# Kernel optimization log

Measured on AMD Instinct MI355X. Metric: run time of the kernel, lower is better.

## Reference

```python
import jax, jax.numpy as jnp
import numpy as np

K = 16  # kNN neighbors (KnnEncoder default)


def _bn(h, g, s):
    # eval-mode BatchNorm with running mean 0 / var 1 folded into affine
    return h * g + s


def setup_inputs() -> dict:
    key = jax.random.key(0)
    cnt = [0]
    def nk():
        cnt[0] += 1
        return jax.random.fold_in(key, cnt[0])
    B, N = 4, 4096
    def W(i, o):
        return jax.random.normal(nk(), (i, o), jnp.float32) / np.float32(i) ** 0.5
    def bias(d):
        return jnp.zeros((d,), jnp.float32)
    def gamma(d):
        return jnp.ones((d,), jnp.float32) + 0.1 * jax.random.normal(nk(), (d,), jnp.float32)
    def beta(d):
        return 0.1 * jax.random.normal(nk(), (d,), jnp.float32)
    inp = dict(
        pos=jax.random.normal(nk(), (B, N, 3), jnp.float32),
        query_point_idx=jax.random.randint(nk(), (B,), 0, N),
        # PointNetConv local MLP: 6 -> 64 -> 128 -> 256 (plain last)
        cw1=W(6, 64), cb1=bias(64), cg1=gamma(64), cs1=beta(64),
        cw2=W(64, 128), cb2=bias(128), cg2=gamma(128), cs2=beta(128),
        cw3=W(128, 256), cb3=bias(256),
        # GlobalSAModule MLP: 259 -> 256 -> 512 -> 1024 (plain last)
        sw1=W(259, 256), sb1=bias(256), sg1=gamma(256), ss1=beta(256),
        sw2=W(256, 512), sb2=bias(512), sg2=gamma(512), ss2=beta(512),
        sw3=W(512, 1024), sb3=bias(1024),
        # EdgeGraspPredictor: 1280 -> 512 -> 256 -> 16
        pw1=W(1280, 512), pb1=bias(512),
        pw2=W(512, 256), pb2=bias(256),
        pw3=W(256, 16), pb3=bias(16),
    )
    return inp


def reference(pos, query_point_idx, cw1, cb1, cg1, cs1, cw2, cb2, cg2, cs2, cw3, cb3,
              sw1, sb1, sg1, ss1, sw2, sb2, sg2, ss2, sw3, sb3,
              pw1, pb1, pw2, pb2, pw3, pb3):
    B, N, _ = pos.shape
    # kNN within each cloud (self included, as torch_geometric knn with x==y)
    d2 = jnp.sum((pos[:, :, None, :] - pos[:, None, :, :]) ** 2, axis=-1)  # [B,N,N]
    _, idx = jax.lax.top_k(-d2, K)  # [B,N,K] targets for each source point n
    nbr = jax.vmap(lambda p, i: p[i])(pos, idx)  # [B,N,K,3] target positions
    # PointNetConv message: cat([x_j = pos_src, pos_src - pos_tgt])
    src = jnp.broadcast_to(pos[:, :, None, :], (B, N, K, 3))
    h = jnp.concatenate([src, src - nbr], axis=-1)  # [B,N,K,6]
    h = jnp.maximum(_bn(h @ cw1 + cb1, cg1, cs1), 0.0)
    h = jnp.maximum(_bn(h @ cw2 + cb2, cg2, cs2), 0.0)
    m = h @ cw3 + cb3  # [B,N,K,256] per-edge messages
    # scatter-max aggregation at target nodes (every node has its self edge)
    tgt = (idx + (jnp.arange(B) * N)[:, None, None]).reshape(-1)
    x = jax.ops.segment_max(m.reshape(-1, m.shape[-1]), tgt, num_segments=B * N)
    x = x.reshape(B, N, -1)  # [B,N,256] per-point features
    # GlobalSAModule: pointwise MLP then global max pool per cloud
    g = jnp.concatenate([x, pos], axis=-1)  # [B,N,259]
    g = jnp.maximum(_bn(g @ sw1 + sb1, sg1, ss1), 0.0)
    g = jnp.maximum(_bn(g @ sw2 + sb2, sg2, ss2), 0.0)
    g = g @ sw3 + sb3  # [B,N,1024]
    scene = jnp.max(g, axis=1)  # [B,1024]
    # gather query point feature, concat with scene feature, predictor MLP
    q = query_point_idx + jnp.arange(B) * N
    point_feat = x.reshape(B * N, -1)[q]  # [B,256]
    ef = jnp.concatenate([point_feat, scene], axis=-1)  # [B,1280]
    h = jnp.maximum(ef @ pw1 + pb1, 0.0)
    h = jnp.maximum(h @ pw2 + pb2, 0.0)
    return h @ pw3 + pb3  # [B,16]
```

## Files before the change

### kernel.cpp

```cpp
#include <hip/hip_runtime.h>

#define BB 4
#define NN 4096
#define KK 16

typedef unsigned short u16;
typedef unsigned int   u32;
typedef unsigned long long u64;

typedef __attribute__((ext_vector_type(8))) short bf16x8;
typedef __attribute__((ext_vector_type(4))) float f32x4;

__device__ __forceinline__ float b2f(u16 x){ return __uint_as_float(((u32)x) << 16); }
__device__ __forceinline__ u16 f2b(float f){
    u32 u = __float_as_uint(f);
    u32 r = (u + 0x7FFFu + ((u >> 16) & 1u)) >> 16;
    return (u16)r;
}
__device__ __forceinline__ u32 fmap(float f){
    u32 u = __float_as_uint(f);
    return (u & 0x80000000u) ? ~u : (u | 0x80000000u);
}
__device__ __forceinline__ float funmap(u32 u){
    u32 v = (u & 0x80000000u) ? (u ^ 0x80000000u) : ~u;
    return __uint_as_float(v);
}

#define N_ARR 27
__device__ const int ASZ[N_ARR] = {
    49152, 384, 64, 64, 64, 8192, 128, 128, 128, 32768, 256,
    66304, 256, 256, 256, 131072, 512, 512, 512, 524288, 1024,
    655360, 512, 131072, 256, 4096, 16 };
__device__ const int AOFF[N_ARR] = {
    0, 49152, 49536, 49600, 49664, 49728, 57920, 58048, 58176, 58304, 91072,
    91328, 157632, 157888, 158144, 158400, 289472, 289984, 290496, 291008, 815296,
    816320, 1471680, 1472192, 1603264, 1603520, 1607616 };

struct Ptrs { const void* p[N_ARR]; };

#define O_POS 0
#define O_CW1 49152
#define O_CB1 49536
#define O_CG1 49600
#define O_CS1 49664
#define O_CB2 57920
#define O_CG2 58048
#define O_CS2 58176
#define O_CB3 91072
#define O_SW1 91328
#define O_SB1 157632
#define O_SG1 157888
#define O_SS1 158144
#define O_SB2 289472
#define O_SG2 289984
#define O_SS2 290496
#define O_SB3 815296
#define O_PW1 816320
#define O_PB1 1471680
#define O_PW2 1472192
#define O_PB2 1603264
#define O_PW3 1603520
#define O_PB3 1607616

__global__ void detect_kernel(const u16* __restrict__ pos_u16, u32* __restrict__ flag){
    __shared__ int cnt;
    if (threadIdx.x == 0) cnt = 0;
    __syncthreads();
    int c = 0;
    #pragma unroll
    for (int s = 0; s < 4; ++s){
        u16 u = pos_u16[2*(threadIdx.x*4 + s)];
        int e = (u >> 7) & 0xFF;
        c += (e >= 0x68 && e <= 0x82) ? 1 : 0;
    }
    atomicAdd(&cnt, c);
    __syncthreads();
    if (threadIdx.x == 0) *flag = (cnt >= 512) ? 1u : 0u;
}

__device__ __forceinline__ void pack_one_src(const void* __restrict__ src, bool isbf,
                                             u16* __restrict__ dst, int tot, int log2n,
                                             int g, int T){
    const int nmask = (1 << log2n) - 1;
    for (int id = g; id < tot; id += T){
        int i = id & 7, lg = (id >> 3) & 3;
        int rest = id >> 5;
        int n = rest & nmask;
        int ks = rest >> log2n;
        int si = (ks*32 + lg*8 + i) << log2n | n;
        dst[id] = isbf ? ((const u16*)src)[si] : f2b(((const float*)src)[si]);
    }
}

__global__ __launch_bounds__(256) void prep_kernel(Ptrs pt, const u32* __restrict__ flagp,
        float* __restrict__ dst, float* __restrict__ psoa,
        u16* __restrict__ wp2, u16* __restrict__ wp3,
        u16* __restrict__ swp1, u16* __restrict__ swp2, u16* __restrict__ swp3){
    const bool isbf = (*flagp != 0);
    const int T = gridDim.x * 256;
    const int g = blockIdx.x * 256 + threadIdx.x;
    #pragma unroll
    for (int a = 0; a < N_ARR; ++a){
        if (a == 5 || a == 9 || a == 15 || a == 19) continue;
        const int sz = ASZ[a], off = AOFF[a];
        if (isbf){
            const u16* s = (const u16*)pt.p[a];
            for (int i = g; i < sz; i += T) dst[off + i] = b2f(s[i]);
        } else {
            const float* s = (const float*)pt.p[a];
            for (int i = g; i < sz; i += T) dst[off + i] = s[i];
        }
    }
    for (int i = g; i < BB*NN; i += T){
        float x, y, z;
        if (isbf){
            const u16* s = (const u16*)pt.p[0];
            x = b2f(s[3*i]); y = b2f(s[3*i+1]); z = b2f(s[3*i+2]);
        } else {
            const float* s = (const float*)pt.p[0];
            x = s[3*i]; y = s[3*i+1]; z = s[3*i+2];
        }
        psoa[i] = x; psoa[BB*NN + i] = y; psoa[2*BB*NN + i] = z;
    }
    pack_one_src(pt.p[5],  isbf, wp2,    8192,  7, g, T);
    pack_one_src(pt.p[9],  isbf, wp3,   32768,  8, g, T);
    pack_one_src(pt.p[11], isbf, swp1,  65536,  8, g, T);
    pack_one_src(pt.p[15], isbf, swp2, 131072,  9, g, T);
    pack_one_src(pt.p[19], isbf, swp3, 524288, 10, g, T);
}

__global__ __launch_bounds__(1024) void sort1_kernel(const float* __restrict__ psoa,
                                                     u64* __restrict__ keys){
    __shared__ u64 s[2048];
    const int half = blockIdx.x;
    const int b    = half >> 1;
    const int base = (half & 1) << 11;
    const float* px = psoa + b*NN;
    const int tid = threadIdx.x;
    for (int i = tid; i < 2048; i += 1024)
        s[i] = (((u64)fmap(px[base + i])) << 32) | (u32)(base + i);
    __syncthreads();
    for (int ksz = 2; ksz <= 2048; ksz <<= 1){
        for (int jj = ksz >> 1; jj > 0; jj >>= 1){
            int t = tid;
            int i  = ((t & ~(jj-1)) << 1) | (t & (jj-1));
            int ix = i | jj;
            u64 a = s[i], v = s[ix];
            bool up = (((base + i) & ksz) == 0);
            if ((a > v) == up){ s[i] = v; s[ix] = a; }
            __syncthreads();
        }
    }
    for (int i = tid; i < 2048; i += 1024) keys[b*NN + base + i] = s[i];
}

__global__ __launch_bounds__(1024) void sort2_kernel(const u64* __restrict__ keys,
        const float* __restrict__ psoa,
        float* __restrict__ xs, float* __restrict__ ys, float* __restrict__ zs,
        int* __restrict__ sidx){
    __shared__ u64 s[NN];
    const int b = blockIdx.x;
    const int tid = threadIdx.x;
    for (int i = tid; i < NN; i += 1024) s[i] = keys[b*NN + i];
    __syncthreads();
    for (int jj = NN >> 1; jj > 0; jj >>= 1){
        for (int t = tid; t < NN/2; t += 1024){
            int i  = ((t & ~(jj-1)) << 1) | (t & (jj-1));
            int ix = i | jj;
            u64 a = s[i], v = s[ix];
            if (a > v){ s[i] = v; s[ix] = a; }
        }
        __syncthreads();
    }
    const float* py = psoa + BB*NN;
    const float* pz = psoa + 2*BB*NN;
    for (int r = tid; r < NN; r += 1024){
        u64 kv = s[r];
        int oi = (int)(u32)(kv & 0xFFFFFFFFu);
        xs[b*NN + r] = funmap((u32)(kv >> 32));
        ys[b*NN + r] = py[b*NN + oi];
        zs[b*NN + r] = pz[b*NN + oi];
        sidx[b*NN + r] = oi;
    }
}

#define QCAP 192
__device__ __forceinline__ void refine16(u64* __restrict__ buf, int& cnt, float& tau, int lane){
    u64 loc[3];
    #pragma unroll
    for (int q = 0; q < 3; ++q){
        int p = lane + (q << 6);
        loc[q] = (p < cnt) ? buf[p] : ~0ull;
    }
    u64 m = ~0ull;
    #pragma unroll
    for (int r = 0; r < KK; ++r){
        m = loc[0];
        m = loc[1] < m ? loc[1] : m;
        m = loc[2] < m ? loc[2] : m;
        #pragma unroll
        for (int off = 32; off > 0; off >>= 1){
            u64 o = __shfl_xor(m, off);
            m = o < m ? o : m;
        }
        if (lane == r) buf[r] = m;
        #pragma unroll
        for (int q = 0; q < 3; ++q) if (loc[q] == m) loc[q] = ~0ull;
    }
    cnt = KK;
    tau = __uint_as_float((u32)(m >> 32));
}

__global__ __launch_bounds__(512) void knn_kernel(
        const float* __restrict__ xs, const float* __restrict__ ys,
        const float* __restrict__ zs, const int* __restrict__ sidx,
        int* __restrict__ knn_out, u32* __restrict__ deg){
    __shared__ __align__(16) u64 kbuf[16*QCAP];
    const int b  = blockIdx.x >> 8;
    const int r0 = (blockIdx.x & 255) << 4;
    const float* X = xs + b*NN;
    const float* Y = ys + b*NN;
    const float* Z = zs + b*NN;
    const int*   S = sidx + b*NN;
    const int tid = threadIdx.x;
    const int lane = tid & 63;
    const int wv = tid >> 6;
    const int rA = r0 + wv*2, rB = rA + 1;
    const float axq = X[rA], ayq = Y[rA], azq = Z[rA];
    const float bxq = X[rB], byq = Y[rB], bzq = Z[rB];
    u64* bufA = kbuf + (wv*2)*QCAP;
    u64* bufB = bufA + QCAP;

    float tauA = 3.0e38f, tauB = 3.0e38f;
    int cntA = 0, cntB = 0;
    for (int k = 0; k < 128; ++k){
        int j = (lane < 32) ? (rA - 1 - (k << 5) - lane)
                            : (rA + (k << 5) + (lane - 32));
        bool inr = ((u32)j < (u32)NN);
        int ja = inr ? j : rA;
        float cx = X[ja], cy = Y[ja], cz = Z[ja];
        float dxA = axq - cx, dyA = ayq - cy, dzA = azq - cz;
        float d2A = __fadd_rn(__fadd_rn(__fmul_rn(dxA,dxA), __fmul_rn(dyA,dyA)), __fmul_rn(dzA,dzA));
        float dxB = bxq - cx, dyB = byq - cy, dzB = bzq - cz;
        float d2B = __fadd_rn(__fadd_rn(__fmul_rn(dxB,dxB), __fmul_rn(dyB,dyB)), __fmul_rn(dzB,dzB));
        bool pA = inr && (d2A <= tauA);
        bool pB = inr && (d2B <= tauB);
        u64 balA = __ballot(pA);
        u64 balB = __ballot(pB);
        int sorig = 0;
        if (balA | balB) sorig = S[ja];
        if (balA){
            int nins = __popcll(balA);
            if (cntA + nins > QCAP) refine16(bufA, cntA, tauA, lane);
            if (pA){
                int ofs = __popcll(balA & ((1ull << lane) - 1ull));
                bufA[cntA + ofs] = (((u64)__float_as_uint(d2A)) << 32) | (u32)sorig;
            }
            cntA += nins;
        }
        if (balB){
            int nins = __popcll(balB);
            if (cntB + nins > QCAP) refine16(bufB, cntB, tauB, lane);
            if (pB){
                int ofs = __popcll(balB & ((1ull << lane) - 1ull));
                bufB[cntB + ofs] = (((u64)__float_as_uint(d2B)) << 32) | (u32)sorig;
            }
            cntB += nins;
        }
        float xL = __shfl(cx, 31);
        float xR = __shfl(cx, 63);
        bool lex = (rA - ((k + 1) << 5) - 1) < 0;
        bool rex = (rA + ((k + 1) << 5)) >= NN;
        float dLa = axq - xL, dRa = xR - axq;
        float dLb = bxq - xL, dRb = xR - bxq;
        bool ldone = lex || (dLa*dLa > tauA && dLb*dLb > tauB);
        bool rdone = rex || (dRa*dRa > tauA && dRb*dRb > tauB);
        if (ldone && rdone) break;
    }
    refine16(bufA, cntA, tauA, lane);
    refine16(bufB, cntB, tauB, lane);
    const int origA = S[rA], origB = S[rB];
    if (lane < KK){
        u64 kA = bufA[lane];
        int jA = (int)(u32)(kA & 0xFFFFFFFFu);
        knn_out[((size_t)(b*NN + origA))*KK + lane] = jA;
        atomicAdd(deg + (b << 12) + jA, 1u);
        u64 kB = bufB[lane];
        int jB = (int)(u32)(kB & 0xFFFFFFFFu);
        knn_out[((size_t)(b*NN + origB))*KK + lane] = jB;
        atomicAdd(deg + (b << 12) + jB, 1u);
    }
}

__global__ __launch_bounds__(1024) void scan_kernel(const u32* __restrict__ deg,
                                                    int* __restrict__ rowstart, u32* __restrict__ cursor){
    __shared__ int lsum[1024];
    const int tid = threadIdx.x;
    const int base = tid * 16;
    int loc[16]; int s = 0;
    #pragma unroll
    for (int q = 0; q < 16; ++q){ loc[q] = (int)deg[base+q]; s += loc[q]; }
    lsum[tid] = s;
    __syncthreads();
    int acc = s;
    for (int ofs = 1; ofs < 1024; ofs <<= 1){
        int t = (tid >= ofs) ? lsum[tid-ofs] : 0;
        __syncthreads();
        acc += t; lsum[tid] = acc;
        __syncthreads();
    }
    int excl = acc - s;
    #pragma unroll
    for (int q = 0; q < 16; ++q){
        rowstart[base+q] = excl; cursor[base+q] = (u32)excl; excl += loc[q];
    }
    if (tid == 1023) rowstart[16384] = excl;
}

__global__ __launch_bounds__(256) void fill_kernel(const int* __restrict__ knn,
                                                   u32* __restrict__ cursor, int* __restrict__ csr){
    int e = blockIdx.x*256 + threadIdx.x;
    int b = e >> 16;
    int t = (b << 12) + knn[e];
    u32 pos = atomicAdd(cursor + t, 1u);
    csr[pos] = e;
}

__device__ __forceinline__ bf16x8 ldfrag(const u16* h, int row, int kofs, int rowstride){
    u32 byte = (u32)((row*rowstride + kofs)*2) ^ (u32)((row & 7) << 4);
    return *(const bf16x8*)((const char*)h + byte);
}
__device__ __forceinline__ void st16(u16* h, int row, int col, int rowstride, float v){
    u32 byte = (u32)((row*rowstride + col)*2) ^ (u32)((row & 7) << 4);
    *(u16*)((char*)h + byte) = f2b(v);
}

__global__ __launch_bounds__(256, 2) void edge_kernel(
    const float* __restrict__ conv, const int* __restrict__ knn,
    const int* __restrict__ rowstart, const int* __restrict__ csr,
    const u16* __restrict__ wp2, const u16* __restrict__ wp3,
    u16* __restrict__ xh)
{
    __shared__ float in6[6][64];
    __shared__ int   lts[64];
    __shared__ int   rs_l[17];
    __shared__ float scw1[384];
    __shared__ float sc1[64], sh1[64];
    __shared__ __align__(16) u16 h1s[64*64];
    __shared__ __align__(16) u16 h2s[64*128];
    __shared__ u32 lsx[16*256];

    const float* posf = conv + O_POS;
    const float* cb1 = conv + O_CB1; const float* cg1 = conv + O_CG1; const float* cs1 = conv + O_CS1;

    const int tid = threadIdx.x;
    const int w   = tid >> 6;
    const int l   = tid & 63;
    const int t0  = blockIdx.x << 4;
    const int b   = t0 >> 12;

    if (tid < 64){ float g1 = cg1[tid]; sc1[tid]=g1; sh1[tid]=cb1[tid]*g1 + cs1[tid]; }
    if (tid < 17) rs_l[tid] = rowstart[t0 + tid];
    for (int u = tid; u < 384; u += 256) scw1[u] = conv[O_CW1 + u];
    #pragma unroll
    for (int q = 0; q < 16; ++q) lsx[q*256 + tid] = 0u;

    const int lr = l & 15, lg = l >> 4;
    const int colb2 = w << 5;
    const int colb3 = w << 6;

    float sc2v[2], sh2v[2], bs3v[4];
    #pragma unroll
    for (int nt = 0; nt < 2; ++nt){
        int c = colb2 + nt*16 + lr;
        float g2 = conv[O_CG2 + c];
        sc2v[nt] = g2; sh2v[nt] = conv[O_CB2 + c]*g2 + conv[O_CS2 + c];
    }
    #pragma unroll
    for (int nt = 0; nt < 4; ++nt) bs3v[nt] = conv[O_CB3 + colb3 + nt*16 + lr];

    __syncthreads();
    const int segstart = rs_l[0], segend = rs_l[16];
    const int nchunk = (segend - segstart + 63) >> 6;

    int curl = -1;
    float run[4];
    #pragma unroll
    for (int nt = 0; nt < 4; ++nt) run[nt] = 0.f;

    for (int ch = 0; ch < nchunk; ++ch){
        __syncthreads();
        if (tid < 64){
            int gpos = segstart + (ch << 6) + tid;
            int lt = -1;
            float ax=0,ay=0,az=0,dx=0,dy=0,dz=0;
            if (gpos < segend){
                lt = 0;
                #pragma unroll
                for (int q = 1; q < 16; ++q) lt += (gpos >= rs_l[q]) ? 1 : 0;
                int e = csr[gpos];
                int i = (e >> 4) & (NN - 1);
                int j = knn[e];
                const float* pi = posf + ((size_t)(b*NN + i))*3;
                const float* pj = posf + ((size_t)(b*NN + j))*3;
                ax = pi[0]; ay = pi[1]; az = pi[2];
                dx = ax - pj[0]; dy = ay - pj[1]; dz = az - pj[2];
            }
            lts[tid] = lt;
            in6[0][tid]=ax; in6[1][tid]=ay; in6[2][tid]=az;
            in6[3][tid]=dx; in6[4][tid]=dy; in6[5][tid]=dz;
        }
        __syncthreads();

        {
            const int e = tid & 63, c0g = (tid >> 6) << 4;
            float a0=in6[0][e], a1=in6[1][e], a2=in6[2][e],
                  a3=in6[3][e], a4=in6[4][e], a5=in6[5][e];
            u32 pk[8];
            #pragma unroll
            for (int ci = 0; ci < 16; ++ci){
                int cc = c0g + ci;
                float acc = a0*scw1[cc]     + a1*scw1[64+cc]  + a2*scw1[128+cc]
                          + a3*scw1[192+cc] + a4*scw1[256+cc] + a5*scw1[320+cc];
                float v = fmaxf(acc*sc1[cc] + sh1[cc], 0.f);
                u32 h = (u32)f2b(v);
                if (ci & 1) pk[ci >> 1] |= h << 16; else pk[ci >> 1] = h;
            }
            u32 base = (u32)(e*128 + c0g*2);
            u32 swz  = (u32)((e & 7) << 4);
            *(uint4*)((char*)h1s + (base ^ swz))        = make_uint4(pk[0],pk[1],pk[2],pk[3]);
            *(uint4*)((char*)h1s + ((base + 16) ^ swz)) = make_uint4(pk[4],pk[5],pk[6],pk[7]);
        }
        __syncthreads();

        {
            f32x4 acc2[4][2];
            #pragma unroll
            for (int mt = 0; mt < 4; ++mt)
                #pragma unroll
                for (int nt = 0; nt < 2; ++nt) acc2[mt][nt] = (f32x4){0.f,0.f,0.f,0.f};
            #pragma unroll
            for (int ks = 0; ks < 2; ++ks){
                bf16x8 bf[2];
                #pragma unroll
                for (int nt = 0; nt < 2; ++nt)
                    bf[nt] = *(const bf16x8*)(wp2 + (((ks*128 + colb2 + nt*16 + lr) << 2) + lg)*8);
                #pragma unroll
                for (int mt = 0; mt < 4; ++mt){
                    bf16x8 a = ldfrag(h1s, mt*16 + lr, ks*32 + lg*8, 64);
                    #pragma unroll
                    for (int nt = 0; nt < 2; ++nt)
                        acc2[mt][nt] = __builtin_amdgcn_mfma_f32_16x16x32_bf16(a, bf[nt], acc2[mt][nt], 0, 0, 0);
                }
            }
            #pragma unroll
            for (int mt = 0; mt < 4; ++mt)
                #pragma unroll
                for (int nt = 0; nt < 2; ++nt)
                    #pragma unroll
                    for (int r = 0; r < 4; ++r){
                        int row = mt*16 + lg*4 + r;
                        float v = fmaxf(acc2[mt][nt][r]*sc2v[nt] + sh2v[nt], 0.f);
                        st16(h2s, row, colb2 + nt*16 + lr, 128, v);
                    }
        }
        __syncthreads();

        {
            f32x4 acc3[4][4];
            #pragma unroll
            for (int mt = 0; mt < 4; ++mt)
                #pragma unroll
                for (int nt = 0; nt < 4; ++nt) acc3[mt][nt] = (f32x4){0.f,0.f,0.f,0.f};
            #pragma unroll
            for (int ks = 0; ks < 4; ++ks){
                bf16x8 bf[4];
                #pragma unroll
                for (int nt = 0; nt < 4; ++nt)
                    bf[nt] = *(const bf16x8*)(wp3 + (((ks*256 + colb3 + nt*16 + lr) << 2) + lg)*8);
                #pragma unroll
                for (int mt = 0; mt < 4; ++mt){
                    bf16x8 a = ldfrag(h2s, mt*16 + lr, ks*32 + lg*8, 128);
                    #pragma unroll
                    for (int nt = 0; nt < 4; ++nt)
                        acc3[mt][nt] = __builtin_amdgcn_mfma_f32_16x16x32_bf16(a, bf[nt], acc3[mt][nt], 0, 0, 0);
                }
            }
            #pragma unroll
            for (int mt = 0; mt < 4; ++mt)
                #pragma unroll
                for (int r = 0; r < 4; ++r){
                    int row = mt*16 + lg*4 + r;
                    int lt = lts[row];
                    if (lt != curl){
                        if (curl >= 0){
                            #pragma unroll
                            for (int nt = 0; nt < 4; ++nt)
                                atomicMax(&lsx[curl*256 + colb3 + nt*16 + lr], fmap(run[nt]));
                        }
                        curl = lt;
                        #pragma unroll
                        for (int nt = 0; nt < 4; ++nt) run[nt] = acc3[mt][nt][r] + bs3v[nt];
                    } else {
                        #pragma unroll
                        for (int nt = 0; nt < 4; ++nt) run[nt] = fmaxf(run[nt], acc3[mt][nt][r] + bs3v[nt]);
                    }
                }
        }
    }
    if (curl >= 0){
        #pragma unroll
        for (int nt = 0; nt < 4; ++nt)
            atomicMax(&lsx[curl*256 + colb3 + nt*16 + lr], fmap(run[nt]));
    }
    __syncthreads();
    #pragma unroll
    for (int q = 0; q < 16; ++q)
        xh[((size_t)(t0+q))*256 + tid] = f2b(funmap(lsx[q*256 + tid]));
}

__global__ __launch_bounds__(256, 3) void sa_kernel(
    const float* __restrict__ conv, const u16* __restrict__ xh,
    const u16* __restrict__ swp1, const u16* __restrict__ swp2, const u16* __restrict__ swp3,
    u32* __restrict__ scene_map)
{
    __shared__ __align__(16) u16 h1s[32*256];
    __shared__ __align__(16) u16 h2s[32*512];
    __shared__ float spw[3][256];
    __shared__ float spx[32], spy[32], spz[32];

    const int tid = threadIdx.x;
    const int w   = tid >> 6;
    const int l   = tid & 63;
    const int lr  = l & 15, lg = l >> 4;
    const int b   = blockIdx.x >> 7;
    const int n0  = (blockIdx.x & 127) << 5;
    const u16* xrow = xh + ((size_t)(b*NN + n0))*256;

    if (tid < 96){
        int p = tid & 31, d = tid >> 5;
        float v = conv[O_POS + ((size_t)(b*NN + n0 + p))*3 + d];
        if (d == 0) spx[p] = v; else if (d == 1) spy[p] = v; else spz[p] = v;
    }
    for (int u = tid; u < 768; u += 256)
        spw[u >> 8][u & 255] = conv[O_SW1 + (256 + (u >> 8))*256 + (u & 255)];
    __syncthreads();

    {
        const int c0 = w << 6;
        float sc1v[4], sh1v[4];
        #pragma unroll
        for (int nt = 0; nt < 4; ++nt){
            int cc = c0 + nt*16 + lr;
            float g = conv[O_SG1 + cc];
            sc1v[nt] = g; sh1v[nt] = conv[O_SB1 + cc]*g + conv[O_SS1 + cc];
        }
        f32x4 acc[2][4];
        #pragma unroll
        for (int mt = 0; mt < 2; ++mt)
            #pragma unroll
            for (int nt = 0; nt < 4; ++nt)
                #pragma unroll
                for (int r = 0; r < 4; ++r){
                    int row = mt*16 + lg*4 + r;
                    int cc  = c0 + nt*16 + lr;
                    acc[mt][nt][r] = spx[row]*spw[0][cc] + spy[row]*spw[1][cc] + spz[row]*spw[2][cc];
                }
        #pragma unroll
        for (int ks = 0; ks < 8; ++ks){
            bf16x8 bf[4];
            #pragma unroll
            for (int nt = 0; nt < 4; ++nt)
                bf[nt] = *(const bf16x8*)(swp1 + (((ks*256 + c0 + nt*16 + lr) << 2) + lg)*8);
            #pragma unroll
            for (int mt = 0; mt < 2; ++mt){
                bf16x8 a = *(const bf16x8*)(xrow + (mt*16 + lr)*256 + ks*32 + lg*8);
                #pragma unroll
                for (int nt = 0; nt < 4; ++nt)
                    acc[mt][nt] = __builtin_amdgcn_mfma_f32_16x16x32_bf16(a, bf[nt], acc[mt][nt], 0, 0, 0);
            }
        }
        #pragma unroll
        for (int mt = 0; mt < 2; ++mt)
            #pragma unroll
            for (int nt = 0; nt < 4; ++nt)
                #pragma unroll
                for (int r = 0; r < 4; ++r){
                    int row = mt*16 + lg*4 + r;
                    float v = fmaxf(acc[mt][nt][r]*sc1v[nt] + sh1v[nt], 0.f);
                    st16(h1s, row, c0 + nt*16 + lr, 256, v);
                }
    }
    __syncthreads();

    {
        const int c0 = w << 7;
        float sc2v[8], sh2v[8];
        #pragma unroll
        for (int nt = 0; nt < 8; ++nt){
            int cc = c0 + nt*16 + lr;
            float g = conv[O_SG2 + cc];
            sc2v[nt] = g; sh2v[nt] = conv[O_SB2 + cc]*g + conv[O_SS2 + cc];
        }
        f32x4 acc[2][8];
        #pragma unroll
        for (int mt = 0; mt < 2; ++mt)
            #pragma unroll
            for (int nt = 0; nt < 8; ++nt) acc[mt][nt] = (f32x4){0.f,0.f,0.f,0.f};
        #pragma unroll
        for (int ks = 0; ks < 8; ++ks){
            bf16x8 bf[8];
            #pragma unroll
            for (int nt = 0; nt < 8; ++nt)
                bf[nt] = *(const bf16x8*)(swp2 + (((ks*512 + c0 + nt*16 + lr) << 2) + lg)*8);
            #pragma unroll
            for (int mt = 0; mt < 2; ++mt){
                bf16x8 a = ldfrag(h1s, mt*16 + lr, ks*32 + lg*8, 256);
                #pragma unroll
                for (int nt = 0; nt < 8; ++nt)
                    acc[mt][nt] = __builtin_amdgcn_mfma_f32_16x16x32_bf16(a, bf[nt], acc[mt][nt], 0, 0, 0);
            }
        }
        #pragma unroll
        for (int mt = 0; mt < 2; ++mt)
            #pragma unroll
            for (int nt = 0; nt < 8; ++nt)
                #pragma unroll
                for (int r = 0; r < 4; ++r){
                    int row = mt*16 + lg*4 + r;
                    float v = fmaxf(acc[mt][nt][r]*sc2v[nt] + sh2v[nt], 0.f);
                    st16(h2s, row, c0 + nt*16 + lr, 512, v);
                }
    }
    __syncthreads();

    #pragma unroll
    for (int half = 0; half < 2; ++half){
        const int c0 = (half << 9) + (w << 7);
        f32x4 acc[2][8];
        #pragma unroll
        for (int mt = 0; mt < 2; ++mt)
            #pragma unroll
            for (int nt = 0; nt < 8; ++nt) acc[mt][nt] = (f32x4){0.f,0.f,0.f,0.f};
        #pragma unroll
        for (int ks = 0; ks < 16; ++ks){
            bf16x8 bf[8];
            #pragma unroll
            for (int nt = 0; nt < 8; ++nt)
                bf[nt] = *(const bf16x8*)(swp3 + (((ks*1024 + c0 + nt*16 + lr) << 2) + lg)*8);
            #pragma unroll
            for (int mt = 0; mt < 2; ++mt){
                bf16x8 a = ldfrag(h2s, mt*16 + lr, ks*32 + lg*8, 512);
                #pragma unroll
                for (int nt = 0; nt < 8; ++nt)
                    acc[mt][nt] = __builtin_amdgcn_mfma_f32_16x16x32_bf16(a, bf[nt], acc[mt][nt], 0, 0, 0);
            }
        }
        #pragma unroll
        for (int nt = 0; nt < 8; ++nt){
            float v = acc[0][nt][0];
            #pragma unroll
            for (int mt = 0; mt < 2; ++mt)
                #pragma unroll
                for (int r = 0; r < 4; ++r) v = fmaxf(v, acc[mt][nt][r]);
            v = fmaxf(v, __shfl_xor(v, 16));
            v = fmaxf(v, __shfl_xor(v, 32));
            if (lg == 0){
                int cc = c0 + nt*16 + lr;
                atomicMax(scene_map + (b << 10) + cc, fmap(v + conv[O_SB3 + cc]));
            }
        }
    }
}

__global__ __launch_bounds__(128) void head1_kernel(
    const float* __restrict__ conv,
    const u16* __restrict__ xh, const u32* __restrict__ scene_map, const int* __restrict__ qidx,
    float* __restrict__ h1out)
{
    __shared__ float ef[1280];
    __shared__ float psum[4][32];
    const float* pw1 = conv + O_PW1; const float* pb1 = conv + O_PB1;
    const int b  = blockIdx.x >> 4;
    const int c0 = (blockIdx.x & 15) << 5;
    const int tid = threadIdx.x;
    const int q = qidx[b];
    for (int u = tid; u < 1280; u += 128){
        float v;
        if (u < 256) v = b2f(xh[(((size_t)(b*NN + q)) << 8) + u]);
        else         v = funmap(scene_map[(b << 10) + (u - 256)]);
        ef[u] = v;
    }
    __syncthreads();
    const int c = c0 + (tid & 31);
    const int rc = tid >> 5;
    float acc = 0.f;
    for (int r = rc*320; r < rc*320 + 320; ++r) acc += ef[r] * pw1[r*512 + c];
    psum[rc][tid & 31] = acc;
    __syncthreads();
    if (tid < 32){
        float a = psum[0][tid] + psum[1][tid] + psum[2][tid] + psum[3][tid] + pb1[c0 + tid];
        h1out[(b << 9) + c0 + tid] = fmaxf(a, 0.f);
    }
}

__global__ __launch_bounds__(256) void head2_kernel(
    const float* __restrict__ conv, const float* __restrict__ h1in,
    const u32* __restrict__ flagp, void* __restrict__ outv)
{
    __shared__ float h1[4][512];
    __shared__ float h2[4][256];
    const float* pw2 = conv + O_PW2; const float* pb2 = conv + O_PB2;
    const float* pw3 = conv + O_PW3; const float* pb3 = conv + O_PB3;
    const int tid = threadIdx.x;
    for (int u = tid; u < 2048; u += 256) h1[u >> 9][u & 511] = h1in[u];
    __syncthreads();
    for (int o = tid; o < 1024; o += 256){
        int b = o >> 8, c = o & 255;
        float acc = pb2[c];
        for (int r = 0; r < 512; ++r) acc += h1[b][r] * pw2[r*256 + c];
        h2[b][c] = fmaxf(acc, 0.f);
    }
    __syncthreads();
    if (tid < 64){
        int b = tid >> 4, c = tid & 15;
        float acc = pb3[c];
        for (int r = 0; r < 256; ++r) acc += h2[b][r] * pw3[r*16 + c];
        if (*flagp) ((u16*)outv)[tid] = f2b(acc);
        else        ((float*)outv)[tid] = acc;
    }
}

extern "C" void kernel_launch(void* const* d_in, const int* in_sizes, int n_in,
                              void* d_out, int out_size, void* d_ws, size_t ws_size,
                              hipStream_t stream){
    (void)in_sizes; (void)n_in; (void)out_size; (void)ws_size;
    const int* qidx = (const int*)d_in[1];

    char* ws = (char*)d_ws;
    u32*  flag      = (u32*)ws;
    float* conv     = (float*)(ws + 1024);
    u16*  wp2       = (u16*)(ws + 6432768);
    u16*  wp3       = (u16*)(ws + 6449152);
    u16*  swp1      = (u16*)(ws + 6514688);
    u16*  swp2      = (u16*)(ws + 6645760);
    u16*  swp3      = (u16*)(ws + 6907904);
    int*  knn       = (int*)(ws + 7956480);
    u32*  deg       = (u32*)(ws + 9005056);
    u32*  scene_map = (u32*)(ws + 9070592);
    int*  rowstart  = (int*)(ws + 9086976);
    u32*  cursor    = (u32*)(ws + 9152576);
    int*  csr       = (int*)(ws + 9218112);
    u16*  xh        = (u16*)(ws + 10266688);
    float* h1ws     = (float*)(ws + 18655296);
    float* psoa     = (float*)(ws + 18663488);
    float* xs       = (float*)(ws + 18860096);
    float* ys       = (float*)(ws + 18925632);
    float* zs       = (float*)(ws + 18991168);
    int*   sidx     = (int*)(ws + 19056704);
    u64*   keys     = (u64*)(ws + 19122240);

    Ptrs pt;
    pt.p[0] = d_in[0];
    for (int k = 1; k < N_ARR; ++k) pt.p[k] = d_in[k + 1];

    hipMemsetAsync(ws + 9005056, 0, 81920, stream);

    detect_kernel <<<1, 256, 0, stream>>>((const u16*)d_in[0], flag);
    prep_kernel   <<<512, 256, 0, stream>>>(pt, flag, conv, psoa, wp2, wp3, swp1, swp2, swp3);
    sort1_kernel  <<<BB*2, 1024, 0, stream>>>(psoa, keys);
    sort2_kernel  <<<BB, 1024, 0, stream>>>(keys, psoa, xs, ys, zs, sidx);
    knn_kernel <<<1024, 512, 0, stream>>>(xs, ys, zs, sidx, knn, deg);
    scan_kernel<<<1, 1024, 0, stream>>>(deg, rowstart, cursor);
    fill_kernel<<<1024, 256, 0, stream>>>(knn, cursor, csr);
    edge_kernel<<<1024, 256, 0, stream>>>(conv, knn, rowstart, csr, wp2, wp3, xh);
    sa_kernel  <<<512, 256, 0, stream>>>(conv, xh, swp1, swp2, swp3, scene_map);
    head1_kernel<<<64, 128, 0, stream>>>(conv, xh, scene_map, qidx, h1ws);
    head2_kernel<<<1, 256, 0, stream>>>(conv, h1ws, flag, (void*)d_out);
}
```

Before: 384.1 us.

## Batch kNN candidate loads per 8 steps and halve SA kernel row tile

The kNN scan now loads 8 candidate chunks of coordinates up front before processing them, so global load latency overlaps instead of stalling on each iteration. The early-exit check now runs only every 8 chunks, so some wasted distance work past the stopping point is possible. The SA kernel tile shrinks from 32 to 16 points per block, doubling the grid to 1024 blocks and raising the occupancy hint to 4 blocks per SIMD-group. This lowers register and LDS use, but each weight fragment is now reused over half as many rows, so weight reads from L2 roughly double.

```diff
diff --git a/kernel.cpp b/kernel.cpp
--- a/kernel.cpp
+++ b/kernel.cpp
@@ -233,42 +233,56 @@
 
     float tauA = 3.0e38f, tauB = 3.0e38f;
     int cntA = 0, cntB = 0;
-    for (int k = 0; k < 128; ++k){
-        int j = (lane < 32) ? (rA - 1 - (k << 5) - lane)
-                            : (rA + (k << 5) + (lane - 32));
-        bool inr = ((u32)j < (u32)NN);
-        int ja = inr ? j : rA;
-        float cx = X[ja], cy = Y[ja], cz = Z[ja];
-        float dxA = axq - cx, dyA = ayq - cy, dzA = azq - cz;
-        float d2A = __fadd_rn(__fadd_rn(__fmul_rn(dxA,dxA), __fmul_rn(dyA,dyA)), __fmul_rn(dzA,dzA));
-        float dxB = bxq - cx, dyB = byq - cy, dzB = bzq - cz;
-        float d2B = __fadd_rn(__fadd_rn(__fmul_rn(dxB,dxB), __fmul_rn(dyB,dyB)), __fmul_rn(dzB,dzB));
-        bool pA = inr && (d2A <= tauA);
-        bool pB = inr && (d2B <= tauB);
-        u64 balA = __ballot(pA);
-        u64 balB = __ballot(pB);
-        int sorig = 0;
-        if (balA | balB) sorig = S[ja];
-        if (balA){
-            int nins = __popcll(balA);
-            if (cntA + nins > QCAP) refine16(bufA, cntA, tauA, lane);
-            if (pA){
-                int ofs = __popcll(balA & ((1ull << lane) - 1ull));
-                bufA[cntA + ofs] = (((u64)__float_as_uint(d2A)) << 32) | (u32)sorig;
-            }
-            cntA += nins;
-        }
-        if (balB){
-            int nins = __popcll(balB);
-            if (cntB + nins > QCAP) refine16(bufB, cntB, tauB, lane);
-            if (pB){
-                int ofs = __popcll(balB & ((1ull << lane) - 1ull));
-                bufB[cntB + ofs] = (((u64)__float_as_uint(d2B)) << 32) | (u32)sorig;
-            }
-            cntB += nins;
-        }
-        float xL = __shfl(cx, 31);
-        float xR = __shfl(cx, 63);
+    for (int k0 = 0; k0 < 128; k0 += 8){
+        float cxv[8], cyv[8], czv[8];
+        #pragma unroll
+        for (int c = 0; c < 8; ++c){
+            int k = k0 + c;
+            int j = (lane < 32) ? (rA - 1 - (k << 5) - lane)
+                                : (rA + (k << 5) + (lane - 32));
+            int ja = ((u32)j < (u32)NN) ? j : rA;
+            cxv[c] = X[ja]; cyv[c] = Y[ja]; czv[c] = Z[ja];
+        }
+        #pragma unroll
+        for (int c = 0; c < 8; ++c){
+            int k = k0 + c;
+            int j = (lane < 32) ? (rA - 1 - (k << 5) - lane)
+                                : (rA + (k << 5) + (lane - 32));
+            bool inr = ((u32)j < (u32)NN);
+            int ja = inr ? j : rA;
+            float cx = cxv[c], cy = cyv[c], cz = czv[c];
+            float dxA = axq - cx, dyA = ayq - cy, dzA = azq - cz;
+            float d2A = __fadd_rn(__fadd_rn(__fmul_rn(dxA,dxA), __fmul_rn(dyA,dyA)), __fmul_rn(dzA,dzA));
+            float dxB = bxq - cx, dyB = byq - cy, dzB = bzq - cz;
+            float d2B = __fadd_rn(__fadd_rn(__fmul_rn(dxB,dxB), __fmul_rn(dyB,dyB)), __fmul_rn(dzB,dzB));
+            bool pA = inr && (d2A <= tauA);
+            bool pB = inr && (d2B <= tauB);
+            u64 balA = __ballot(pA);
+            u64 balB = __ballot(pB);
+            int sorig = 0;
+            if (balA | balB) sorig = S[ja];
+            if (balA){
+                int nins = __popcll(balA);
+                if (cntA + nins > QCAP) refine16(bufA, cntA, tauA, lane);
+                if (pA){
+                    int ofs = __popcll(balA & ((1ull << lane) - 1ull));
+                    bufA[cntA + ofs] = (((u64)__float_as_uint(d2A)) << 32) | (u32)sorig;
+                }
+                cntA += nins;
+            }
+            if (balB){
+                int nins = __popcll(balB);
+                if (cntB + nins > QCAP) refine16(bufB, cntB, tauB, lane);
+                if (pB){
+                    int ofs = __popcll(balB & ((1ull << lane) - 1ull));
+                    bufB[cntB + ofs] = (((u64)__float_as_uint(d2B)) << 32) | (u32)sorig;
+                }
+                cntB += nins;
+            }
+        }
+        float xL = __shfl(cxv[7], 31);
+        float xR = __shfl(cxv[7], 63);
+        const int k = k0 + 7;
         bool lex = (rA - ((k + 1) << 5) - 1) < 0;
         bool rex = (rA + ((k + 1) << 5)) >= NN;
         float dLa = axq - xL, dRa = xR - axq;
@@ -519,26 +533,26 @@
         xh[((size_t)(t0+q))*256 + tid] = f2b(funmap(lsx[q*256 + tid]));
 }
 
-__global__ __launch_bounds__(256, 3) void sa_kernel(
+__global__ __launch_bounds__(256, 4) void sa_kernel(
     const float* __restrict__ conv, const u16* __restrict__ xh,
     const u16* __restrict__ swp1, const u16* __restrict__ swp2, const u16* __restrict__ swp3,
     u32* __restrict__ scene_map)
 {
-    __shared__ __align__(16) u16 h1s[32*256];
-    __shared__ __align__(16) u16 h2s[32*512];
+    __shared__ __align__(16) u16 h1s[16*256];
+    __shared__ __align__(16) u16 h2s[16*512];
     __shared__ float spw[3][256];
-    __shared__ float spx[32], spy[32], spz[32];
+    __shared__ float spx[16], spy[16], spz[16];
 
     const int tid = threadIdx.x;
     const int w   = tid >> 6;
     const int l   = tid & 63;
     const int lr  = l & 15, lg = l >> 4;
-    const int b   = blockIdx.x >> 7;
-    const int n0  = (blockIdx.x & 127) << 5;
+    const int b   = blockIdx.x >> 8;
+    const int n0  = (blockIdx.x & 255) << 4;
     const u16* xrow = xh + ((size_t)(b*NN + n0))*256;
 
-    if (tid < 96){
-        int p = tid & 31, d = tid >> 5;
+    if (tid < 48){
+        int p = tid & 15, d = tid >> 4;
         float v = conv[O_POS + ((size_t)(b*NN + n0 + p))*3 + d];
         if (d == 0) spx[p] = v; else if (d == 1) spy[p] = v; else spz[p] = v;
     }
@@ -555,41 +569,34 @@
             float g = conv[O_SG1 + cc];
             sc1v[nt] = g; sh1v[nt] = conv[O_SB1 + cc]*g + conv[O_SS1 + cc];
         }
-        f32x4 acc[2][4];
-        #pragma unroll
-        for (int mt = 0; mt < 2; ++mt)
-            #pragma unroll
-            for (int nt = 0; nt < 4; ++nt)
-                #pragma unroll
-                for (int r = 0; r < 4; ++r){
-                    int row = mt*16 + lg*4 + r;
-                    int cc  = c0 + nt*16 + lr;
-                    acc[mt][nt][r] = spx[row]*spw[0][cc] + spy[row]*spw[1][cc] + spz[row]*spw[2][cc];
-                }
+        f32x4 acc[4];
+        #pragma unroll
+        for (int nt = 0; nt < 4; ++nt)
+            #pragma unroll
+            for (int r = 0; r < 4; ++r){
+                int row = lg*4 + r;
+                int cc  = c0 + nt*16 + lr;
+                acc[nt][r] = spx[row]*spw[0][cc] + spy[row]*spw[1][cc] + spz[row]*spw[2][cc];
+            }
         #pragma unroll
         for (int ks = 0; ks < 8; ++ks){
             bf16x8 bf[4];
             #pragma unroll
             for (int nt = 0; nt < 4; ++nt)
                 bf[nt] = *(const bf16x8*)(swp1 + (((ks*256 + c0 + nt*16 + lr) << 2) + lg)*8);
-            #pragma unroll
-            for (int mt = 0; mt < 2; ++mt){
-                bf16x8 a = *(const bf16x8*)(xrow + (mt*16 + lr)*256 + ks*32 + lg*8);
-                #pragma unroll
-                for (int nt = 0; nt < 4; ++nt)
-                    acc[mt][nt] = __builtin_amdgcn_mfma_f32_16x16x32_bf16(a, bf[nt], acc[mt][nt], 0, 0, 0);
-            }
-        }
-        #pragma unroll
-        for (int mt = 0; mt < 2; ++mt)
+            bf16x8 a = *(const bf16x8*)(xrow + lr*256 + ks*32 + lg*8);
             #pragma unroll
             for (int nt = 0; nt < 4; ++nt)
-                #pragma unroll
-                for (int r = 0; r < 4; ++r){
-                    int row = mt*16 + lg*4 + r;
-                    float v = fmaxf(acc[mt][nt][r]*sc1v[nt] + sh1v[nt], 0.f);
-                    st16(h1s, row, c0 + nt*16 + lr, 256, v);
-                }
+                acc[nt] = __builtin_amdgcn_mfma_f32_16x16x32_bf16(a, bf[nt], acc[nt], 0, 0, 0);
+        }
+        #pragma unroll
+        for (int nt = 0; nt < 4; ++nt)
+            #pragma unroll
+            for (int r = 0; r < 4; ++r){
+                int row = lg*4 + r;
+                float v = fmaxf(acc[nt][r]*sc1v[nt] + sh1v[nt], 0.f);
+                st16(h1s, row, c0 + nt*16 + lr, 256, v);
+            }
     }
     __syncthreads();
 
@@ -602,67 +609,51 @@
             float g = conv[O_SG2 + cc];
             sc2v[nt] = g; sh2v[nt] = conv[O_SB2 + cc]*g + conv[O_SS2 + cc];
         }
-        f32x4 acc[2][8];
-        #pragma unroll
-        for (int mt = 0; mt < 2; ++mt)
-            #pragma unroll
-            for (int nt = 0; nt < 8; ++nt) acc[mt][nt] = (f32x4){0.f,0.f,0.f,0.f};
+        f32x4 acc[8];
+        #pragma unroll
+        for (int nt = 0; nt < 8; ++nt) acc[nt] = (f32x4){0.f,0.f,0.f,0.f};
         #pragma unroll
         for (int ks = 0; ks < 8; ++ks){
             bf16x8 bf[8];
             #pragma unroll
             for (int nt = 0; nt < 8; ++nt)
                 bf[nt] = *(const bf16x8*)(swp2 + (((ks*512 + c0 + nt*16 + lr) << 2) + lg)*8);
-            #pragma unroll
-            for (int mt = 0; mt < 2; ++mt){
-                bf16x8 a = ldfrag(h1s, mt*16 + lr, ks*32 + lg*8, 256);
-                #pragma unroll
-                for (int nt = 0; nt < 8; ++nt)
-                    acc[mt][nt] = __builtin_amdgcn_mfma_f32_16x16x32_bf16(a, bf[nt], acc[mt][nt], 0, 0, 0);
-            }
-        }
-        #pragma unroll
-        for (int mt = 0; mt < 2; ++mt)
+            bf16x8 a = ldfrag(h1s, lr, ks*32 + lg*8, 256);
             #pragma unroll
             for (int nt = 0; nt < 8; ++nt)
-                #pragma unroll
-                for (int r = 0; r < 4; ++r){
-                    int row = mt*16 + lg*4 + r;
-                    float v = fmaxf(acc[mt][nt][r]*sc2v[nt] + sh2v[nt], 0.f);
-                    st16(h2s, row, c0 + nt*16 + lr, 512, v);
-                }
+                acc[nt] = __builtin_amdgcn_mfma_f32_16x16x32_bf16(a, bf[nt], acc[nt], 0, 0, 0);
+        }
+        #pragma unroll
+        for (int nt = 0; nt < 8; ++nt)
+            #pragma unroll
+            for (int r = 0; r < 4; ++r){
+                int row = lg*4 + r;
+                float v = fmaxf(acc[nt][r]*sc2v[nt] + sh2v[nt], 0.f);
+                st16(h2s, row, c0 + nt*16 + lr, 512, v);
+            }
     }
     __syncthreads();
 
     #pragma unroll
     for (int half = 0; half < 2; ++half){
         const int c0 = (half << 9) + (w << 7);
-        f32x4 acc[2][8];
-        #pragma unroll
-        for (int mt = 0; mt < 2; ++mt)
-            #pragma unroll
-            for (int nt = 0; nt < 8; ++nt) acc[mt][nt] = (f32x4){0.f,0.f,0.f,0.f};
+        f32x4 acc[8];
+        #pragma unroll
+        for (int nt = 0; nt < 8; ++nt) acc[nt] = (f32x4){0.f,0.f,0.f,0.f};
         #pragma unroll
         for (int ks = 0; ks < 16; ++ks){
             bf16x8 bf[8];
             #pragma unroll
             for (int nt = 0; nt < 8; ++nt)
                 bf[nt] = *(const bf16x8*)(swp3 + (((ks*1024 + c0 + nt*16 + lr) << 2) + lg)*8);
-            #pragma unroll
-            for (int mt = 0; mt < 2; ++mt){
-                bf16x8 a = ldfrag(h2s, mt*16 + lr, ks*32 + lg*8, 512);
-                #pragma unroll
-                for (int nt = 0; nt < 8; ++nt)
-                    acc[mt][nt] = __builtin_amdgcn_mfma_f32_16x16x32_bf16(a, bf[nt], acc[mt][nt], 0, 0, 0);
-            }
+            bf16x8 a = ldfrag(h2s, lr, ks*32 + lg*8, 512);
+            #pragma unroll
+            for (int nt = 0; nt < 8; ++nt)
+                acc[nt] = __builtin_amdgcn_mfma_f32_16x16x32_bf16(a, bf[nt], acc[nt], 0, 0, 0);
         }
         #pragma unroll
         for (int nt = 0; nt < 8; ++nt){
-            float v = acc[0][nt][0];
-            #pragma unroll
-            for (int mt = 0; mt < 2; ++mt)
-                #pragma unroll
-                for (int r = 0; r < 4; ++r) v = fmaxf(v, acc[mt][nt][r]);
+            float v = fmaxf(fmaxf(acc[nt][0], acc[nt][1]), fmaxf(acc[nt][2], acc[nt][3]));
             v = fmaxf(v, __shfl_xor(v, 16));
             v = fmaxf(v, __shfl_xor(v, 32));
             if (lg == 0){
@@ -774,7 +765,7 @@
     scan_kernel<<<1, 1024, 0, stream>>>(deg, rowstart, cursor);
     fill_kernel<<<1024, 256, 0, stream>>>(knn, cursor, csr);
     edge_kernel<<<1024, 256, 0, stream>>>(conv, knn, rowstart, csr, wp2, wp3, xh);
-    sa_kernel  <<<512, 256, 0, stream>>>(conv, xh, swp1, swp2, swp3, scene_map);
+    sa_kernel  <<<BB*256, 256, 0, stream>>>(conv, xh, swp1, swp2, swp3, scene_map);
     head1_kernel<<<64, 128, 0, stream>>>(conv, xh, scene_map, qidx, h1ws);
     head2_kernel<<<1, 256, 0, stream>>>(conv, h1ws, flag, (void*)d_out);
 }
```

Result: slower. 426.4 us (+11.0%).
